# Performance work log

Measured on AMD Instinct MI355X. Metric: run time of the kernel, lower is better.

## Reference

```python
import jax, jax.numpy as jnp
import numpy as np

N, E, C, L, NG = 50000, 600000, 128, 7, 512
EPS = 1e-7


def layer_norm(z, g, b):
    mu = z.mean(-1, keepdims=True)
    var = ((z - mu) ** 2).mean(-1, keepdims=True)
    return (z - mu) * jax.lax.rsqrt(var + 1e-5) * g + b


def setup_inputs() -> dict:
    key = jax.random.key(0)
    ks = jax.random.split(key, 16)
    inp = {
        'x': jax.random.randint(ks[0], (N, 9), 0, 64, dtype=jnp.int32),
        'edge_index': jax.random.randint(ks[1], (2, E), 0, N, dtype=jnp.int32),
        'edge_attr': jax.random.randint(ks[2], (E, 3), 0, 8, dtype=jnp.int32),
        'batch': jnp.sort(jax.random.randint(ks[3], (N,), 0, NG, dtype=jnp.int32)),
        'atom_emb': jax.random.normal(ks[4], (9, 64, C), jnp.float32) * 0.1,
        'bond_emb': jax.random.normal(ks[5], (3, 8, C), jnp.float32) * 0.1,
        'vn_emb': jnp.zeros((1, C), jnp.float32),
        'conv_W1': jax.random.normal(ks[6], (L, C, 2 * C), jnp.float32) / np.sqrt(C),
        'conv_b1': jnp.zeros((L, 2 * C), jnp.float32),
        'conv_g1': jnp.ones((L, 2 * C), jnp.float32),
        'conv_bb1': jnp.zeros((L, 2 * C), jnp.float32),
        'conv_W2': jax.random.normal(ks[7], (L, 2 * C, C), jnp.float32) / np.sqrt(2 * C),
        'conv_b2': jnp.zeros((L, C), jnp.float32),
        'norm_g': jnp.ones((L, C), jnp.float32),
        'norm_b': jnp.zeros((L, C), jnp.float32),
        'vn_W1': jax.random.normal(ks[8], (L - 1, C, C), jnp.float32) / np.sqrt(C),
        'vn_b1': jnp.zeros((L - 1, C), jnp.float32),
        'vn_g': jnp.ones((L - 1, C), jnp.float32),
        'vn_bb': jnp.zeros((L - 1, C), jnp.float32),
        'vn_W2': jax.random.normal(ks[9], (L - 1, C, C), jnp.float32) / np.sqrt(C),
        'vn_b2': jnp.zeros((L - 1, C), jnp.float32),
    }
    return inp


def reference(x, edge_index, edge_attr, batch, atom_emb, bond_emb, vn_emb,
              conv_W1, conv_b1, conv_g1, conv_bb1, conv_W2, conv_b2,
              norm_g, norm_b, vn_W1, vn_b1, vn_g, vn_bb, vn_W2, vn_b2):
    src, dst = edge_index[0], edge_index[1]

    # AtomEncoder: sum of per-feature embeddings -> [N, C]
    h = atom_emb[jnp.arange(9), x].sum(axis=1)
    # BondEncoder (conv_encode_edge=False) -> [E, C]
    edge_emb = bond_emb[jnp.arange(3), edge_attr].sum(axis=1)

    # virtual node embedding (one per graph)
    vn = jnp.broadcast_to(vn_emb[0], (NG, C))
    h = h + vn[batch]

    def gen_conv(l, hx):
        # GENConv: msg = relu(x_j + e) + eps; softmax aggregation (t=1); MLP(x+m)
        msg = jax.nn.relu(hx[src] + edge_emb) + EPS                      # [E, C]
        mx = jax.ops.segment_max(msg, dst, num_segments=N)               # [N, C]
        e = jnp.exp(msg - mx[dst])
        den = jax.ops.segment_sum(e, dst, num_segments=N)
        m = jax.ops.segment_sum(msg * (e / (den[dst] + 1e-16)), dst, num_segments=N)
        z = hx + m
        z = jax.nn.relu(layer_norm(z @ conv_W1[l] + conv_b1[l], conv_g1[l], conv_bb1[l]))
        return z @ conv_W2[l] + conv_b2[l]

    # res+ block: Conv -> [Norm -> ReLU -> (VN update) -> Conv + res]*
    h = gen_conv(0, h)
    for l in range(1, L):
        h2 = jax.nn.relu(layer_norm(h, norm_g[l - 1], norm_b[l - 1]))
        vtmp = jax.ops.segment_sum(h2, batch, num_segments=NG) + vn
        v = jax.nn.relu(layer_norm(vtmp @ vn_W1[l - 1] + vn_b1[l - 1], vn_g[l - 1], vn_bb[l - 1]))
        vn = v @ vn_W2[l - 1] + vn_b2[l - 1]
        h2 = h2 + vn[batch]
        h = gen_conv(l, h2) + h
    h = layer_norm(h, norm_g[L - 1], norm_b[L - 1])

    # global_add_pool -> [NG, C]
    return jax.ops.segment_sum(h, batch, num_segments=NG)
```

## Files before the change

### kernel.cpp

```cpp
#include <hip/hip_runtime.h>
#include <hip/hip_bf16.h>
#include <stdint.h>

#define N_NODES 50000
#define N_EDGES 600000
#define CH 128
#define NLAYERS 7
#define NGRAPHS 512

typedef __hip_bfloat16 bf16;
using bf16x8 = __attribute__((ext_vector_type(8))) __bf16;
using f32x4  = __attribute__((ext_vector_type(4))) float;
using u32x4  = __attribute__((ext_vector_type(4))) uint32_t;

static __device__ __forceinline__ float b2f(bf16 v){ return __bfloat162float(v); }

static __device__ __forceinline__ void bar_lds(){
  asm volatile("s_waitcnt lgkmcnt(0)" ::: "memory");
  __builtin_amdgcn_sched_barrier(0);
  __builtin_amdgcn_s_barrier();
}

__global__ void k_detect(const uint32_t* __restrict__ g, int* __restrict__ flag){
  if (threadIdx.x == 0 && blockIdx.x == 0) flag[0] = (g[0] == 0x3F803F80u) ? 1 : 0;
}

struct Segs { const void* src[12]; float* dst[12]; int n[12]; };

__global__ void k_cvt_all(const int* __restrict__ flag, Segs S){
  int f = flag[0];
  int seg = blockIdx.y;
  int n = S.n[seg];
  const void* src = S.src[seg];
  float* dst = S.dst[seg];
  for (int i = blockIdx.x*blockDim.x + threadIdx.x; i < n; i += gridDim.x*blockDim.x)
    dst[i] = f ? b2f(((const bf16*)src)[i]) : ((const float*)src)[i];
}

__global__ void k_transpose_all(const int* __restrict__ flag,
    const void* W1, const void* W2, const void* vW1, const void* vW2,
    bf16* W1p, bf16* W2T, bf16* vW1p, bf16* vW2T){
  int f = flag[0];
  const int T0 = NLAYERS*128*256, T1 = NLAYERS*256*128;
  const int T2 = (NLAYERS-1)*128*128;
  int total = T0+T1+2*T2;
  for (int i = blockIdx.x*blockDim.x + threadIdx.x; i < total; i += gridDim.x*blockDim.x){
    float v;
    if (i < T0){
      int idx = i; int l = idx/(128*256); int rem = idx - l*128*256; int k = rem >> 8; int n = rem & 255;
      v = f ? b2f(((const bf16*)W1)[idx]) : ((const float*)W1)[idx];
      W1p[(size_t)l*256*128 + n*128 + (k ^ ((n&7)<<3))] = __float2bfloat16(v);
    } else if (i < T0+T1){
      int idx = i-T0; int l = idx/(256*128); int rem = idx - l*256*128; int k = rem >> 7; int n = rem & 127;
      v = f ? b2f(((const bf16*)W2)[idx]) : ((const float*)W2)[idx];
      W2T[(size_t)l*128*256 + n*256 + k] = __float2bfloat16(v);
    } else if (i < T0+T1+T2){
      int idx = i-T0-T1; int l = idx/(128*128); int rem = idx - l*128*128; int k = rem >> 7; int n = rem & 127;
      v = f ? b2f(((const bf16*)vW1)[idx]) : ((const float*)vW1)[idx];
      vW1p[(size_t)l*128*128 + n*128 + (k ^ ((n&7)<<3))] = __float2bfloat16(v);
    } else {
      int idx = i-T0-T1-T2; int l = idx/(128*128); int rem = idx - l*128*128; int k = rem >> 7; int n = rem & 127;
      v = f ? b2f(((const bf16*)vW2)[idx]) : ((const float*)vW2)[idx];
      vW2T[(size_t)l*128*128 + n*128 + k] = __float2bfloat16(v);
    }
  }
}

__global__ void k_bondC(const int* __restrict__ flag, const void* __restrict__ bond,
                        uint32_t* __restrict__ bondC){
  int i = blockIdx.x*blockDim.x + threadIdx.x;
  if (i >= 512*64) return;
  int f = flag[0];
  int idx = i >> 6, t = i & 63;
  int a0 = idx & 7, a1 = (idx>>3) & 7, a2 = (idx>>6) & 7;
  auto g = [&](int e)->float{ return f ? b2f(((const bf16*)bond)[e]) : ((const float*)bond)[e]; };
  int c0 = 2*t, c1 = 2*t+1;
  float s0 = g((0*8+a0)*128 + c0) + g((1*8+a1)*128 + c0) + g((2*8+a2)*128 + c0);
  float s1 = g((0*8+a0)*128 + c1) + g((1*8+a1)*128 + c1) + g((2*8+a2)*128 + c1);
  __hip_bfloat162 p; p.x = __float2bfloat16(s0); p.y = __float2bfloat16(s1);
  bondC[i] = *reinterpret_cast<uint32_t*>(&p);
}

__global__ void k_zero_i32(int* p, int n){
  for (int i = blockIdx.x*blockDim.x + threadIdx.x; i < n; i += gridDim.x*blockDim.x) p[i] = 0;
}

__global__ void k_hist(const int* __restrict__ keys, int* __restrict__ counts, int n){
  for (int i = blockIdx.x*blockDim.x + threadIdx.x; i < n; i += gridDim.x*blockDim.x)
    atomicAdd(&counts[keys[i]], 1);
}

__global__ __launch_bounds__(256) void k_scanA(const int* __restrict__ in, int* __restrict__ out,
                                               int* __restrict__ bsums, int n){
  __shared__ int lds[256];
  int t = threadIdx.x;
  int base = blockIdx.x * 1024;
  int v[4]; int s = 0;
  #pragma unroll
  for (int i=0;i<4;i++){ int idx = base + t*4 + i; int x = (idx<n)? in[idx] : 0; v[i]=x; s+=x; }
  lds[t] = s; __syncthreads();
  for (int off=1; off<256; off<<=1){
    int x = (t>=off)? lds[t-off] : 0;
    __syncthreads();
    lds[t] += x;
    __syncthreads();
  }
  int p = lds[t] - s;
  #pragma unroll
  for (int i=0;i<4;i++){ int idx = base + t*4 + i; if (idx<n) out[idx] = p; p += v[i]; }
  if (t==255) bsums[blockIdx.x] = lds[255];
}

__global__ __launch_bounds__(256) void k_scanB(int* bsums, int nblk){
  __shared__ int lds[256];
  int t = threadIdx.x;
  int v = (t<nblk)? bsums[t] : 0;
  lds[t] = v; __syncthreads();
  for (int off=1; off<256; off<<=1){
    int x = (t>=off)? lds[t-off] : 0;
    __syncthreads();
    lds[t] += x;
    __syncthreads();
  }
  if (t<nblk) bsums[t] = lds[t] - v;
}

__global__ void k_scanC(int* out, const int* bsums, int n){
  for (int i = blockIdx.x*blockDim.x + threadIdx.x; i < n; i += gridDim.x*blockDim.x)
    out[i] += bsums[i >> 10];
}

__global__ void k_scatter(const int* __restrict__ ei, const int* __restrict__ ea,
                          const int* __restrict__ row_ptr, int* __restrict__ fill,
                          uint32_t* __restrict__ csr){
  for (int e = blockIdx.x*blockDim.x + threadIdx.x; e < N_EDGES; e += gridDim.x*blockDim.x){
    int src = ei[e];
    int dst = ei[N_EDGES + e];
    int pos = row_ptr[dst] + atomicAdd(&fill[dst], 1);
    uint32_t a0 = (uint32_t)ea[e*3+0], a1 = (uint32_t)ea[e*3+1], a2 = (uint32_t)ea[e*3+2];
    csr[pos] = (uint32_t)src | ((a0 | (a1<<3) | (a2<<6)) << 16);
  }
}

__global__ void k_gptr(const int* __restrict__ batch, int* __restrict__ gptr){
  int i = blockIdx.x*blockDim.x + threadIdx.x;
  if (i >= N_NODES) return;
  int b = batch[i];
  if (i == 0){ for (int g=0; g<=b; ++g) gptr[g] = 0; }
  else { int bp = batch[i-1]; for (int g=bp+1; g<=b; ++g) gptr[g] = i; }
  if (i == N_NODES-1){ for (int g=b+1; g<=NGRAPHS; ++g) gptr[g] = N_NODES; }
}

__global__ __launch_bounds__(128) void k_atom_encode(const int* __restrict__ x,
    const float* __restrict__ atom_emb, const float* __restrict__ vn_emb,
    uint32_t* __restrict__ hxb){
  int n = blockIdx.x; int c = threadIdx.x;
  float s = vn_emb[c];
  #pragma unroll
  for (int f=0; f<9; ++f){
    int xv = x[n*9+f];
    s += atom_emb[(f*64 + xv)*CH + c];
  }
  float o = __shfl_xor(s, 1);
  if ((c & 1) == 0){
    __hip_bfloat162 p; p.x = __float2bfloat16(s); p.y = __float2bfloat16(o);
    hxb[n*64 + (c>>1)] = *reinterpret_cast<uint32_t*>(&p);
  }
}

__global__ void k_vn_init(const float* __restrict__ vn_emb, float* __restrict__ vn){
  for (int i = blockIdx.x*blockDim.x + threadIdx.x; i < NGRAPHS*CH; i += gridDim.x*blockDim.x)
    vn[i] = vn_emb[i & (CH-1)];
}

__global__ __launch_bounds__(64) void k_aggregate(const uint32_t* __restrict__ hxb,
     const uint32_t* __restrict__ csr, const int* __restrict__ row_ptr,
     const uint32_t* __restrict__ bondC, uint32_t* __restrict__ z){
  int n = (blockIdx.x & 7)*(N_NODES/8) + (blockIdx.x >> 3);
  int t = threadIdx.x;
  int s0 = row_ptr[n], s1 = row_ptr[n+1];
  float sa=0.f, sb=0.f, wa=0.f, wb=0.f;
  int i = s0;
  for (; i+4 <= s1; i += 4){
    uint32_t u0=csr[i], u1=csr[i+1], u2=csr[i+2], u3=csr[i+3];
    uint32_t h0 = hxb[(size_t)(u0 & 0xFFFFu)*64 + t];
    uint32_t h1 = hxb[(size_t)(u1 & 0xFFFFu)*64 + t];
    uint32_t h2 = hxb[(size_t)(u2 & 0xFFFFu)*64 + t];
    uint32_t h3 = hxb[(size_t)(u3 & 0xFFFFu)*64 + t];
    uint32_t c0 = bondC[(size_t)(u0 >> 16)*64 + t];
    uint32_t c1 = bondC[(size_t)(u1 >> 16)*64 + t];
    uint32_t c2 = bondC[(size_t)(u2 >> 16)*64 + t];
    uint32_t c3 = bondC[(size_t)(u3 >> 16)*64 + t];
    #define EDGE(hp, bc) { \
      float va = __uint_as_float(hp << 16) + __uint_as_float(bc << 16); \
      float vb = __uint_as_float(hp & 0xFFFF0000u) + __uint_as_float(bc & 0xFFFF0000u); \
      va = fmaxf(va, 0.f) + 1e-7f; vb = fmaxf(vb, 0.f) + 1e-7f; \
      float pa = __expf(va - 10.f), pb = __expf(vb - 10.f); \
      sa += pa; wa += pa*va; sb += pb; wb += pb*vb; }
    EDGE(h0, c0) EDGE(h1, c1) EDGE(h2, c2) EDGE(h3, c3)
  }
  for (; i < s1; ++i){
    uint32_t u = csr[i];
    uint32_t hp = hxb[(size_t)(u & 0xFFFFu)*64 + t];
    uint32_t bc = bondC[(size_t)(u >> 16)*64 + t];
    EDGE(hp, bc)
    #undef EDGE
  }
  uint32_t own = hxb[(size_t)n*64 + t];
  float za = __uint_as_float(own << 16)         + wa/(sa + 1e-16f);
  float zb = __uint_as_float(own & 0xFFFF0000u) + wb/(sb + 1e-16f);
  __hip_bfloat162 p; p.x = __float2bfloat16(za); p.y = __float2bfloat16(zb);
  z[(size_t)n*64 + (t ^ ((n&7)<<2))] = *reinterpret_cast<uint32_t*>(&p);
}

template<int K, int N1, int N2, bool VNIN, bool BF16IO>
__global__ __launch_bounds__(512, 2) void k_mlp12(const bf16* __restrict__ A,
    const float* __restrict__ Af32,
    const bf16* __restrict__ W1s,
    const float* __restrict__ b1, const float* __restrict__ g1, const float* __restrict__ bb1,
    const bf16* __restrict__ W2T,
    const float* __restrict__ b2,
    const float* __restrict__ lng, const float* __restrict__ lnb,
    const void* __restrict__ residual, void* __restrict__ out,
    bf16* __restrict__ hxn, int relu2, int M, int NT)
{
  constexpr int KK1 = K/32;
  constexpr int WC  = N1/4;
  constexpr int JC  = WC/16;
  constexpr int KK2 = N1/32;
  __shared__ __align__(16) bf16 W1L[N1*K];
  __shared__ __align__(16) bf16 AL[2][64*K];
  __shared__ __align__(16) bf16 zt[64*N1];
  __shared__ float lnp[64][4][2];
  __shared__ float lnv[64][2];

  const int tid = threadIdx.x;
  const int wid = tid >> 6, lane = tid & 63;
  const int wr = wid >> 2, wc = wid & 3;
  const int rlo = lane & 15, hi = lane >> 4, khi = hi*8;

  {
    constexpr int NC_ = (N1*K*2)/1024/8;
    #pragma unroll
    for (int c=0;c<NC_;++c){
      int cc = c*8 + wid;
      __builtin_amdgcn_global_load_lds((const uint32_t*)((const char*)W1s + cc*1024 + lane*16),
                                       (uint32_t*)((char*)W1L + cc*1024), 16, 0, 0);
    }
  }

  float b1v[JC], gv[JC], bbv[JC];
  #pragma unroll
  for (int jc=0;jc<JC;++jc){
    int col = wc*WC + jc*16 + rlo;
    b1v[jc] = b1[col]; gv[jc] = g1[col]; bbv[jc] = bb1[col];
  }
  float bv2[2] = { b2[wc*32 + rlo], b2[wc*32 + 16 + rlo] };
  float lngv[2] = {0.f,0.f}, lnbv[2] = {0.f,0.f};
  if (hxn){
    lngv[0] = lng[wc*32 + rlo];      lnbv[0] = lnb[wc*32 + rlo];
    lngv[1] = lng[wc*32 + 16 + rlo]; lnbv[1] = lnb[wc*32 + 16 + rlo];
  }
  u32x4 b2raw[2][KK2];
  #pragma unroll
  for (int ct=0;ct<2;++ct){
    const bf16* wp = W2T + (size_t)(wc*32 + ct*16 + rlo)*N1 + khi;
    #pragma unroll
    for (int kk=0;kk<KK2;++kk){
      b2raw[ct][kk] = *reinterpret_cast<const u32x4*>(wp + kk*32);
      asm volatile("" : "+v"(b2raw[ct][kk]));
    }
  }

  auto stageA = [&](int nb, int tile){
    if constexpr (!VNIN){
      const char* src = (const char*)A + (size_t)tile*(64*K*2);
      constexpr int NCA = (64*K*2)/1024/8;
      #pragma unroll
      for (int c=0;c<NCA;++c){
        int cc = c*8 + wid;
        __builtin_amdgcn_global_load_lds((const uint32_t*)(src + cc*1024 + lane*16),
                                         (uint32_t*)((char*)&AL[nb][0] + cc*1024), 16, 0, 0);
      }
    } else {
      int base = tile*64;
      #pragma unroll
      for (int e=0;e<(64*K/4)/512;++e){
        int idx = tid + e*512;
        int row = idx >> 5;
        int k4  = (idx & 31)*4;
        float4 v = *reinterpret_cast<const float4*>(Af32 + (size_t)(base+row)*K + k4);
        int s = (row&7)<<3;
        bf16* d = &AL[nb][row*K + (k4 ^ s)];
        d[0]=__float2bfloat16(v.x); d[1]=__float2bfloat16(v.y);
        d[2]=__float2bfloat16(v.z); d[3]=__float2bfloat16(v.w);
      }
    }
  };

  int t = blockIdx.x, buf = 0;
  stageA(0, t);
  __syncthreads();

  while (true){
    int tn = t + (int)gridDim.x;

    f32x4 acc1[2][JC];
    #pragma unroll
    for (int rt=0;rt<2;++rt)
      #pragma unroll
      for (int jc=0;jc<JC;++jc) acc1[rt][jc] = {0.f,0.f,0.f,0.f};
    #pragma unroll
    for (int kk=0;kk<KK1;++kk){
      bf16x8 af[2], bw[JC];
      #pragma unroll
      for (int rt=0;rt<2;++rt){
        int lr = wr*32 + rt*16 + rlo;
        af[rt] = *reinterpret_cast<const bf16x8*>(&AL[buf][lr*K + ((kk*32 + khi) ^ ((lr&7)<<3))]);
      }
      #pragma unroll
      for (int jc=0;jc<JC;++jc){
        int n = wc*WC + jc*16 + rlo;
        bw[jc] = *reinterpret_cast<const bf16x8*>(&W1L[n*K + ((kk*32 + khi) ^ ((n&7)<<3))]);
      }
      #pragma unroll
      for (int rt=0;rt<2;++rt)
        #pragma unroll
        for (int jc=0;jc<JC;++jc)
          acc1[rt][jc] = __builtin_amdgcn_mfma_f32_16x16x32_bf16(af[rt], bw[jc], acc1[rt][jc], 0,0,0);
    }

    if (tn < NT) stageA(buf^1, tn);
    float resv[2][2][4];
    if (residual){
      #pragma unroll
      for (int rt=0;rt<2;++rt)
        #pragma unroll
        for (int r=0;r<4;++r){
          int grow = t*64 + wr*32 + rt*16 + hi*4 + r; if (grow >= M) grow = M-1;
          #pragma unroll
          for (int ct=0;ct<2;++ct){
            size_t off = (size_t)grow*N2 + wc*32 + ct*16 + rlo;
            resv[rt][ct][r] = BF16IO ? b2f(((const bf16*)residual)[off])
                                     : ((const float*)residual)[off];
          }
        }
    }
    __builtin_amdgcn_sched_barrier(0);

    float p[2][4], q[2][4];
    #pragma unroll
    for (int rt=0;rt<2;++rt)
      #pragma unroll
      for (int r=0;r<4;++r){ p[rt][r]=0.f; q[rt][r]=0.f; }
    #pragma unroll
    for (int jc=0;jc<JC;++jc)
      #pragma unroll
      for (int rt=0;rt<2;++rt)
        #pragma unroll
        for (int r=0;r<4;++r){
          float v = acc1[rt][jc][r] + b1v[jc]; acc1[rt][jc][r] = v;
          p[rt][r] += v; q[rt][r] += v*v;
        }
    #pragma unroll
    for (int rt=0;rt<2;++rt)
      #pragma unroll
      for (int r=0;r<4;++r){
        float pv = p[rt][r], qv = q[rt][r];
        #pragma unroll
        for (int off=1; off<16; off<<=1){ pv += __shfl_xor(pv, off); qv += __shfl_xor(qv, off); }
        if (rlo == 0){
          int row = wr*32 + rt*16 + hi*4 + r;
          lnp[row][wc][0] = pv; lnp[row][wc][1] = qv;
        }
      }
    bar_lds();
    if (tid < 64){
      float P=0.f, Q=0.f;
      #pragma unroll
      for (int w=0;w<4;++w){ P += lnp[tid][w][0]; Q += lnp[tid][w][1]; }
      float mu = P*(1.f/N1);
      lnv[tid][0] = mu;
      lnv[tid][1] = rsqrtf(Q*(1.f/N1) - mu*mu + 1e-5f);
    }
    bar_lds();

    #pragma unroll
    for (int rt=0;rt<2;++rt)
      #pragma unroll
      for (int r=0;r<4;++r){
        int row = wr*32 + rt*16 + hi*4 + r;
        float mu = lnv[row][0], rs = lnv[row][1];
        #pragma unroll
        for (int jc=0;jc<JC;++jc){
          int col = wc*WC + jc*16 + rlo;
          float y = (acc1[rt][jc][r]-mu)*rs*gv[jc] + bbv[jc];
          zt[row*N1 + (col ^ ((row&7)<<3))] = __float2bfloat16(fmaxf(y, 0.f));
        }
      }
    bar_lds();

    f32x4 acc2[2][2];
    #pragma unroll
    for (int rt=0;rt<2;++rt)
      #pragma unroll
      for (int ct=0;ct<2;++ct) acc2[rt][ct] = {0.f,0.f,0.f,0.f};
    #pragma unroll
    for (int kk=0;kk<KK2;++kk){
      bf16x8 a2[2];
      #pragma unroll
      for (int rt=0;rt<2;++rt){
        int row = wr*32 + rt*16 + rlo;
        a2[rt] = *reinterpret_cast<const bf16x8*>(&zt[row*N1 + ((kk*32 + khi) ^ ((row&7)<<3))]);
      }
      #pragma unroll
      for (int rt=0;rt<2;++rt)
        #pragma unroll
        for (int ct=0;ct<2;++ct){
          bf16x8 bb;
          __builtin_memcpy(&bb, &b2raw[ct][kk], 16);
          acc2[rt][ct] = __builtin_amdgcn_mfma_f32_16x16x32_bf16(a2[rt], bb, acc2[rt][ct], 0,0,0);
        }
    }

    float vmat[2][2][4];
    #pragma unroll
    for (int rt=0;rt<2;++rt)
      #pragma unroll
      for (int ct=0;ct<2;++ct)
        #pragma unroll
        for (int r=0;r<4;++r){
          float v = acc2[rt][ct][r] + bv2[ct];
          if (residual) v += resv[rt][ct][r];
          vmat[rt][ct][r] = v;
          int grow = t*64 + wr*32 + rt*16 + hi*4 + r;
          if (grow < M){
            size_t off = (size_t)grow*N2 + wc*32 + ct*16 + rlo;
            if (BF16IO) ((bf16*)out)[off] = __float2bfloat16(v);
            else        ((float*)out)[off] = v;
          }
        }

    if (hxn){
      #pragma unroll
      for (int rt=0;rt<2;++rt)
        #pragma unroll
        for (int r=0;r<4;++r){
          float pv = vmat[rt][0][r] + vmat[rt][1][r];
          float qv = vmat[rt][0][r]*vmat[rt][0][r] + vmat[rt][1][r]*vmat[rt][1][r];
          #pragma unroll
          for (int off=1; off<16; off<<=1){ pv += __shfl_xor(pv, off); qv += __shfl_xor(qv, off); }
          if (rlo == 0){
            int row = wr*32 + rt*16 + hi*4 + r;
            lnp[row][wc][0] = pv; lnp[row][wc][1] = qv;
          }
        }
      bar_lds();
      if (tid < 64){
        float P=0.f, Q=0.f;
        #pragma unroll
        for (int w=0;w<4;++w){ P += lnp[tid][w][0]; Q += lnp[tid][w][1]; }
        float mu = P*(1.f/N2);
        lnv[tid][0] = mu;
        lnv[tid][1] = rsqrtf(Q*(1.f/N2) - mu*mu + 1e-5f);
      }
      bar_lds();
      #pragma unroll
      for (int rt=0;rt<2;++rt)
        #pragma unroll
        for (int r=0;r<4;++r){
          int row = wr*32 + rt*16 + hi*4 + r;
          float mu = lnv[row][0], rs = lnv[row][1];
          int grow = t*64 + row;
          if (grow < M){
            #pragma unroll
            for (int ct=0;ct<2;++ct){
              float y = (vmat[rt][ct][r]-mu)*rs*lngv[ct] + lnbv[ct];
              if (relu2) y = fmaxf(y, 0.f);
              hxn[(size_t)grow*N2 + wc*32 + ct*16 + rlo] = __float2bfloat16(y);
            }
          }
        }
    }

    if (tn >= NT) break;
    t = tn; buf ^= 1;
    __syncthreads();
  }
}

__global__ void k_vncopy(const float* __restrict__ vn, float* __restrict__ vnacc){
  int i = blockIdx.x*blockDim.x + threadIdx.x;
  if (i < NGRAPHS*CH) vnacc[i] = vn[i];
}

#define SEGC 128
__global__ __launch_bounds__(128) void k_segsum2(const bf16* __restrict__ hxn,
    const int* __restrict__ batch, float* __restrict__ vnacc){
  int c = threadIdx.x;
  int n0 = blockIdx.x*SEGC;
  int n1 = n0 + SEGC; if (n1 > N_NODES) n1 = N_NODES;
  if (n0 >= N_NODES) return;
  int cur = batch[n0];
  float s = 0.f;
  for (int n = n0; n < n1; ++n){
    int b = batch[n];
    if (b != cur){ atomicAdd(&vnacc[cur*CH + c], s); s = 0.f; cur = b; }
    s += b2f(hxn[(size_t)n*CH + c]);
  }
  atomicAdd(&vnacc[cur*CH + c], s);
}

__global__ void k_add_vn(const uint32_t* __restrict__ hxn, const float* __restrict__ vn,
                         const int* __restrict__ batch, uint32_t* __restrict__ hxb){
  for (int i = blockIdx.x*blockDim.x + threadIdx.x; i < N_NODES*64; i += gridDim.x*blockDim.x){
    int n = i >> 6; int t = i & 63;
    uint32_t hp = hxn[i];
    float2 vv = *reinterpret_cast<const float2*>(vn + (size_t)batch[n]*CH + 2*t);
    float za = __uint_as_float(hp << 16)         + vv.x;
    float zb = __uint_as_float(hp & 0xFFFF0000u) + vv.y;
    __hip_bfloat162 p; p.x = __float2bfloat16(za); p.y = __float2bfloat16(zb);
    hxb[i] = *reinterpret_cast<uint32_t*>(&p);
  }
}

__global__ __launch_bounds__(128) void k_pool(const bf16* __restrict__ hxn,
    const int* __restrict__ gptr, const int* __restrict__ flag, void* __restrict__ out){
  int g = blockIdx.x; int c = threadIdx.x;
  float s = 0.f;
  for (int n = gptr[g]; n < gptr[g+1]; ++n) s += b2f(hxn[(size_t)n*CH + c]);
  if (flag[0]) ((bf16*)out)[g*CH+c] = __float2bfloat16(s);
  else         ((float*)out)[g*CH+c] = s;
}

extern "C" void kernel_launch(void* const* d_in, const int* in_sizes, int n_in,
                              void* d_out, int out_size, void* d_ws, size_t ws_size,
                              hipStream_t stream)
{
  const int*  x     = (const int*) d_in[0];
  const int*  ei    = (const int*) d_in[1];
  const int*  ea    = (const int*) d_in[2];
  const int*  batch = (const int*) d_in[3];
  const void* atom_emb = d_in[4];
  const void* bond_emb = d_in[5];
  const void* vn_emb   = d_in[6];
  const void* conv_W1  = d_in[7];
  const void* conv_b1  = d_in[8];
  const void* conv_g1  = d_in[9];
  const void* conv_bb1 = d_in[10];
  const void* conv_W2  = d_in[11];
  const void* conv_b2  = d_in[12];
  const void* norm_g   = d_in[13];
  const void* norm_b   = d_in[14];
  const void* vn_W1    = d_in[15];
  const void* vn_b1    = d_in[16];
  const void* vn_g     = d_in[17];
  const void* vn_bb    = d_in[18];
  const void* vn_W2    = d_in[19];
  const void* vn_b2    = d_in[20];

  char* wsb = (char*)d_ws;
  size_t off = 0;
  auto alloc = [&](size_t bytes)->char*{ char* p = wsb + off; off += (bytes + 255) & ~(size_t)255; return p; };
  const int ZROWS = 50048;
  uint32_t* hb    = (uint32_t*)alloc(sizeof(uint32_t)*ZROWS*64);
  uint32_t* hxn   = (uint32_t*)alloc(sizeof(uint32_t)*ZROWS*64);
  uint32_t* hxb   = (uint32_t*)alloc(sizeof(uint32_t)*N_NODES*64);
  uint32_t* z     = (uint32_t*)alloc(sizeof(uint32_t)*ZROWS*64);
  float*    vn    = (float*)   alloc(sizeof(float)*NGRAPHS*CH);
  float*    vnacc = (float*)   alloc(sizeof(float)*NGRAPHS*CH);
  bf16*     W1Tp  = (bf16*)    alloc(sizeof(bf16)*NLAYERS*256*128);
  bf16*     W2T   = (bf16*)    alloc(sizeof(bf16)*NLAYERS*128*256);
  bf16*     vW1Tp = (bf16*)    alloc(sizeof(bf16)*(NLAYERS-1)*128*128);
  bf16*     vW2T  = (bf16*)    alloc(sizeof(bf16)*(NLAYERS-1)*128*128);
  int* row_ptr = (int*)alloc(sizeof(int)*(N_NODES+1));
  int* counts  = (int*)alloc(sizeof(int)*(N_NODES+1));
  uint32_t* csr = (uint32_t*)alloc(sizeof(uint32_t)*N_EDGES);
  int* gptr    = (int*)alloc(sizeof(int)*(NGRAPHS+1));
  int* bsums   = (int*)alloc(sizeof(int)*256);
  int* flag    = (int*)alloc(sizeof(int)*64);
  float* atomF = (float*)alloc(sizeof(float)*9*64*CH);
  uint32_t* bondC = (uint32_t*)alloc(sizeof(uint32_t)*512*64);
  float* vnEF  = (float*)alloc(sizeof(float)*CH);
  float* b1F   = (float*)alloc(sizeof(float)*NLAYERS*2*CH);
  float* g1F   = (float*)alloc(sizeof(float)*NLAYERS*2*CH);
  float* bb1F  = (float*)alloc(sizeof(float)*NLAYERS*2*CH);
  float* b2F   = (float*)alloc(sizeof(float)*NLAYERS*CH);
  float* ngF   = (float*)alloc(sizeof(float)*NLAYERS*CH);
  float* nbF   = (float*)alloc(sizeof(float)*NLAYERS*CH);
  float* vb1F  = (float*)alloc(sizeof(float)*(NLAYERS-1)*CH);
  float* vgF   = (float*)alloc(sizeof(float)*(NLAYERS-1)*CH);
  float* vbbF  = (float*)alloc(sizeof(float)*(NLAYERS-1)*CH);
  float* vb2F  = (float*)alloc(sizeof(float)*(NLAYERS-1)*CH);

  k_detect<<<1, 64, 0, stream>>>((const uint32_t*)norm_g, flag);
  Segs S;
  int si = 0;
  auto seg = [&](const void* s_, float* d_, int n_){ S.src[si]=s_; S.dst[si]=d_; S.n[si]=n_; ++si; };
  seg(atom_emb, atomF, 9*64*CH);
  seg(vn_emb,   vnEF,  CH);
  seg(conv_b1,  b1F,  NLAYERS*2*CH);
  seg(conv_g1,  g1F,  NLAYERS*2*CH);
  seg(conv_bb1, bb1F, NLAYERS*2*CH);
  seg(conv_b2,  b2F,  NLAYERS*CH);
  seg(norm_g,   ngF,  NLAYERS*CH);
  seg(norm_b,   nbF,  NLAYERS*CH);
  seg(vn_b1,    vb1F, (NLAYERS-1)*CH);
  seg(vn_g,     vgF,  (NLAYERS-1)*CH);
  seg(vn_bb,    vbbF, (NLAYERS-1)*CH);
  seg(vn_b2,    vb2F, (NLAYERS-1)*CH);
  k_cvt_all<<<dim3(72, 12), 256, 0, stream>>>(flag, S);
  k_transpose_all<<<640, 256, 0, stream>>>(flag, conv_W1, conv_W2, vn_W1, vn_W2,
                                           W1Tp, W2T, vW1Tp, vW2T);
  k_bondC<<<128, 256, 0, stream>>>(flag, bond_emb, bondC);

  k_zero_i32<<<64, 256, 0, stream>>>(counts, N_NODES+1);
  k_hist<<<512, 256, 0, stream>>>(ei + N_EDGES, counts, N_EDGES);
  int nblkE = (N_NODES+1 + 1023)/1024;
  k_scanA<<<nblkE, 256, 0, stream>>>(counts, row_ptr, bsums, N_NODES+1);
  k_scanB<<<1, 256, 0, stream>>>(bsums, nblkE);
  k_scanC<<<64, 256, 0, stream>>>(row_ptr, bsums, N_NODES+1);
  k_zero_i32<<<64, 256, 0, stream>>>(counts, N_NODES+1);
  k_scatter<<<512, 256, 0, stream>>>(ei, ea, row_ptr, counts, csr);
  k_gptr<<<(N_NODES+255)/256, 256, 0, stream>>>(batch, gptr);

  k_atom_encode<<<N_NODES, 128, 0, stream>>>(x, atomF, vnEF, hxb);
  k_vn_init<<<64, 256, 0, stream>>>(vnEF, vn);

  const int NT_CONV = (N_NODES + 63)/64;
  const int NT_VN   = NGRAPHS/64;

  for (int l = 0; l < NLAYERS; ++l){
    if (l > 0){
      k_vncopy<<<(NGRAPHS*CH+255)/256, 256, 0, stream>>>(vn, vnacc);
      k_segsum2<<<(N_NODES+SEGC-1)/SEGC, 128, 0, stream>>>((const bf16*)hxn, batch, vnacc);
      k_mlp12<128,128,128,true,false><<<NT_VN, 512, 0, stream>>>(nullptr, vnacc,
          vW1Tp + (size_t)(l-1)*128*128, vb1F + (l-1)*CH, vgF + (l-1)*CH, vbbF + (l-1)*CH,
          vW2T + (size_t)(l-1)*128*128, vb2F + (l-1)*CH,
          nullptr, nullptr, nullptr, vn, nullptr, 0, NGRAPHS, NT_VN);
      k_add_vn<<<1024, 256, 0, stream>>>(hxn, vn, batch, hxb);
    }
    k_aggregate<<<N_NODES, 64, 0, stream>>>(hxb, csr, row_ptr, bondC, z);
    k_mlp12<128,256,128,false,true><<<256, 512, 0, stream>>>((const bf16*)z, nullptr,
        W1Tp + (size_t)l*256*128, b1F + l*2*CH, g1F + l*2*CH, bb1F + l*2*CH,
        W2T + (size_t)l*128*256, b2F + l*CH,
        ngF + l*CH, nbF + l*CH,
        (l==0)? nullptr : (const void*)hb, (void*)hb, (bf16*)hxn,
        (l < NLAYERS-1) ? 1 : 0, N_NODES, NT_CONV);
  }
  k_pool<<<NGRAPHS, 128, 0, stream>>>((const bf16*)hxn, gptr, flag, d_out);
}
```

Before: 952.6 us.

## Fuse edge softmax aggregation into the conv MLP kernel

The separate per-node aggregation kernel is removed. Each 64-row tile of the conv MLP kernel now computes its own softmax-weighted neighbour aggregation directly into shared memory, with 8 rows per wave, before running the two GEMMs and layernorms. This drops the z intermediate write and read and one launch per layer. In exchange, the gather latency is no longer overlapped by a double-buffered A stage, and the 256 persistent blocks at 2 per CU may hide memory latency less well than the old 50000 small blocks. The VN MLP path is split off into its own simplified kernel.

```diff
diff --git a/kernel.cpp b/kernel.cpp
--- a/kernel.cpp
+++ b/kernel.cpp
@@ -173,56 +173,290 @@
     vn[i] = vn_emb[i & (CH-1)];
 }
 
-__global__ __launch_bounds__(64) void k_aggregate(const uint32_t* __restrict__ hxb,
-     const uint32_t* __restrict__ csr, const int* __restrict__ row_ptr,
-     const uint32_t* __restrict__ bondC, uint32_t* __restrict__ z){
-  int n = (blockIdx.x & 7)*(N_NODES/8) + (blockIdx.x >> 3);
-  int t = threadIdx.x;
-  int s0 = row_ptr[n], s1 = row_ptr[n+1];
-  float sa=0.f, sb=0.f, wa=0.f, wb=0.f;
-  int i = s0;
-  for (; i+4 <= s1; i += 4){
-    uint32_t u0=csr[i], u1=csr[i+1], u2=csr[i+2], u3=csr[i+3];
-    uint32_t h0 = hxb[(size_t)(u0 & 0xFFFFu)*64 + t];
-    uint32_t h1 = hxb[(size_t)(u1 & 0xFFFFu)*64 + t];
-    uint32_t h2 = hxb[(size_t)(u2 & 0xFFFFu)*64 + t];
-    uint32_t h3 = hxb[(size_t)(u3 & 0xFFFFu)*64 + t];
-    uint32_t c0 = bondC[(size_t)(u0 >> 16)*64 + t];
-    uint32_t c1 = bondC[(size_t)(u1 >> 16)*64 + t];
-    uint32_t c2 = bondC[(size_t)(u2 >> 16)*64 + t];
-    uint32_t c3 = bondC[(size_t)(u3 >> 16)*64 + t];
-    #define EDGE(hp, bc) { \
-      float va = __uint_as_float(hp << 16) + __uint_as_float(bc << 16); \
-      float vb = __uint_as_float(hp & 0xFFFF0000u) + __uint_as_float(bc & 0xFFFF0000u); \
-      va = fmaxf(va, 0.f) + 1e-7f; vb = fmaxf(vb, 0.f) + 1e-7f; \
-      float pa = __expf(va - 10.f), pb = __expf(vb - 10.f); \
-      sa += pa; wa += pa*va; sb += pb; wb += pb*vb; }
-    EDGE(h0, c0) EDGE(h1, c1) EDGE(h2, c2) EDGE(h3, c3)
-  }
-  for (; i < s1; ++i){
-    uint32_t u = csr[i];
-    uint32_t hp = hxb[(size_t)(u & 0xFFFFu)*64 + t];
-    uint32_t bc = bondC[(size_t)(u >> 16)*64 + t];
-    EDGE(hp, bc)
-    #undef EDGE
-  }
-  uint32_t own = hxb[(size_t)n*64 + t];
-  float za = __uint_as_float(own << 16)         + wa/(sa + 1e-16f);
-  float zb = __uint_as_float(own & 0xFFFF0000u) + wb/(sb + 1e-16f);
-  __hip_bfloat162 p; p.x = __float2bfloat16(za); p.y = __float2bfloat16(zb);
-  z[(size_t)n*64 + (t ^ ((n&7)<<2))] = *reinterpret_cast<uint32_t*>(&p);
-}
-
-template<int K, int N1, int N2, bool VNIN, bool BF16IO>
-__global__ __launch_bounds__(512, 2) void k_mlp12(const bf16* __restrict__ A,
-    const float* __restrict__ Af32,
+template<int K, int N1, int N2>
+__global__ __launch_bounds__(512, 2) void k_mlp13(
+    const uint32_t* __restrict__ hxb,
+    const uint32_t* __restrict__ csr, const int* __restrict__ row_ptr,
+    const uint32_t* __restrict__ bondC,
     const bf16* __restrict__ W1s,
     const float* __restrict__ b1, const float* __restrict__ g1, const float* __restrict__ bb1,
     const bf16* __restrict__ W2T,
     const float* __restrict__ b2,
     const float* __restrict__ lng, const float* __restrict__ lnb,
-    const void* __restrict__ residual, void* __restrict__ out,
+    const bf16* __restrict__ residual, bf16* __restrict__ out,
     bf16* __restrict__ hxn, int relu2, int M, int NT)
+{
+  constexpr int KK1 = K/32;
+  constexpr int WC  = N1/4;
+  constexpr int JC  = WC/16;
+  constexpr int KK2 = N1/32;
+  __shared__ __align__(16) bf16 W1L[N1*K];
+  __shared__ __align__(16) bf16 AL[64*K];
+  __shared__ __align__(16) bf16 zt[64*N1];
+  __shared__ float lnp[64][4][2];
+  __shared__ float lnv[64][2];
+
+  const int tid = threadIdx.x;
+  const int wid = tid >> 6, lane = tid & 63;
+  const int wr = wid >> 2, wc = wid & 3;
+  const int rlo = lane & 15, hi = lane >> 4, khi = hi*8;
+
+  {
+    constexpr int NC_ = (N1*K*2)/1024/8;
+    #pragma unroll
+    for (int c=0;c<NC_;++c){
+      int cc = c*8 + wid;
+      __builtin_amdgcn_global_load_lds((const uint32_t*)((const char*)W1s + cc*1024 + lane*16),
+                                       (uint32_t*)((char*)W1L + cc*1024), 16, 0, 0);
+    }
+  }
+
+  float b1v[JC], gv[JC], bbv[JC];
+  #pragma unroll
+  for (int jc=0;jc<JC;++jc){
+    int col = wc*WC + jc*16 + rlo;
+    b1v[jc] = b1[col]; gv[jc] = g1[col]; bbv[jc] = bb1[col];
+  }
+  float bv2[2] = { b2[wc*32 + rlo], b2[wc*32 + 16 + rlo] };
+  float lngv[2] = { lng[wc*32 + rlo], lng[wc*32 + 16 + rlo] };
+  float lnbv[2] = { lnb[wc*32 + rlo], lnb[wc*32 + 16 + rlo] };
+  u32x4 b2raw[2][KK2];
+  #pragma unroll
+  for (int ct=0;ct<2;++ct){
+    const bf16* wp = W2T + (size_t)(wc*32 + ct*16 + rlo)*N1 + khi;
+    #pragma unroll
+    for (int kk=0;kk<KK2;++kk){
+      b2raw[ct][kk] = *reinterpret_cast<const u32x4*>(wp + kk*32);
+      asm volatile("" : "+v"(b2raw[ct][kk]));
+    }
+  }
+
+  uint32_t* AL32 = (uint32_t*)AL;
+
+  for (int t = blockIdx.x; ; t += (int)gridDim.x){
+    #pragma unroll 1
+    for (int j=0;j<8;++j){
+      int row = wid*8 + j;
+      int n = t*64 + row;
+      uint32_t res = 0;
+      if (n < M){
+        int s0 = row_ptr[n], s1 = row_ptr[n+1];
+        float sa=0.f, sb=0.f, wa=0.f, wb=0.f;
+        int i = s0;
+        for (; i+4 <= s1; i += 4){
+          uint32_t u0=csr[i], u1=csr[i+1], u2=csr[i+2], u3=csr[i+3];
+          uint32_t h0 = hxb[(size_t)(u0 & 0xFFFFu)*64 + lane];
+          uint32_t h1 = hxb[(size_t)(u1 & 0xFFFFu)*64 + lane];
+          uint32_t h2 = hxb[(size_t)(u2 & 0xFFFFu)*64 + lane];
+          uint32_t h3 = hxb[(size_t)(u3 & 0xFFFFu)*64 + lane];
+          uint32_t c0 = bondC[(size_t)(u0 >> 16)*64 + lane];
+          uint32_t c1 = bondC[(size_t)(u1 >> 16)*64 + lane];
+          uint32_t c2 = bondC[(size_t)(u2 >> 16)*64 + lane];
+          uint32_t c3 = bondC[(size_t)(u3 >> 16)*64 + lane];
+          #define EDGE(hp, bc) { \
+            float va = __uint_as_float(hp << 16) + __uint_as_float(bc << 16); \
+            float vb = __uint_as_float(hp & 0xFFFF0000u) + __uint_as_float(bc & 0xFFFF0000u); \
+            va = fmaxf(va, 0.f) + 1e-7f; vb = fmaxf(vb, 0.f) + 1e-7f; \
+            float pa = __expf(va - 10.f), pb = __expf(vb - 10.f); \
+            sa += pa; wa += pa*va; sb += pb; wb += pb*vb; }
+          EDGE(h0, c0) EDGE(h1, c1) EDGE(h2, c2) EDGE(h3, c3)
+        }
+        for (; i < s1; ++i){
+          uint32_t u = csr[i];
+          uint32_t hp = hxb[(size_t)(u & 0xFFFFu)*64 + lane];
+          uint32_t bc = bondC[(size_t)(u >> 16)*64 + lane];
+          EDGE(hp, bc)
+          #undef EDGE
+        }
+        uint32_t own = hxb[(size_t)n*64 + lane];
+        float za = __uint_as_float(own << 16)         + wa/(sa + 1e-16f);
+        float zb = __uint_as_float(own & 0xFFFF0000u) + wb/(sb + 1e-16f);
+        __hip_bfloat162 p; p.x = __float2bfloat16(za); p.y = __float2bfloat16(zb);
+        res = *reinterpret_cast<uint32_t*>(&p);
+      }
+      AL32[row*(K/2) + (lane ^ ((row&7)<<2))] = res;
+    }
+    __syncthreads();
+
+    f32x4 acc1[2][JC];
+    #pragma unroll
+    for (int rt=0;rt<2;++rt)
+      #pragma unroll
+      for (int jc=0;jc<JC;++jc) acc1[rt][jc] = {0.f,0.f,0.f,0.f};
+    #pragma unroll
+    for (int kk=0;kk<KK1;++kk){
+      bf16x8 af[2], bw[JC];
+      #pragma unroll
+      for (int rt=0;rt<2;++rt){
+        int lr = wr*32 + rt*16 + rlo;
+        af[rt] = *reinterpret_cast<const bf16x8*>(&AL[lr*K + ((kk*32 + khi) ^ ((lr&7)<<3))]);
+      }
+      #pragma unroll
+      for (int jc=0;jc<JC;++jc){
+        int n = wc*WC + jc*16 + rlo;
+        bw[jc] = *reinterpret_cast<const bf16x8*>(&W1L[n*K + ((kk*32 + khi) ^ ((n&7)<<3))]);
+      }
+      #pragma unroll
+      for (int rt=0;rt<2;++rt)
+        #pragma unroll
+        for (int jc=0;jc<JC;++jc)
+          acc1[rt][jc] = __builtin_amdgcn_mfma_f32_16x16x32_bf16(af[rt], bw[jc], acc1[rt][jc], 0,0,0);
+    }
+
+    float resv[2][2][4];
+    if (residual){
+      #pragma unroll
+      for (int rt=0;rt<2;++rt)
+        #pragma unroll
+        for (int r=0;r<4;++r){
+          int grow = t*64 + wr*32 + rt*16 + hi*4 + r; if (grow >= M) grow = M-1;
+          #pragma unroll
+          for (int ct=0;ct<2;++ct)
+            resv[rt][ct][r] = b2f(residual[(size_t)grow*N2 + wc*32 + ct*16 + rlo]);
+        }
+    }
+    __builtin_amdgcn_sched_barrier(0);
+
+    float p[2][4], q[2][4];
+    #pragma unroll
+    for (int rt=0;rt<2;++rt)
+      #pragma unroll
+      for (int r=0;r<4;++r){ p[rt][r]=0.f; q[rt][r]=0.f; }
+    #pragma unroll
+    for (int jc=0;jc<JC;++jc)
+      #pragma unroll
+      for (int rt=0;rt<2;++rt)
+        #pragma unroll
+        for (int r=0;r<4;++r){
+          float v = acc1[rt][jc][r] + b1v[jc]; acc1[rt][jc][r] = v;
+          p[rt][r] += v; q[rt][r] += v*v;
+        }
+    #pragma unroll
+    for (int rt=0;rt<2;++rt)
+      #pragma unroll
+      for (int r=0;r<4;++r){
+        float pv = p[rt][r], qv = q[rt][r];
+        #pragma unroll
+        for (int off=1; off<16; off<<=1){ pv += __shfl_xor(pv, off); qv += __shfl_xor(qv, off); }
+        if (rlo == 0){
+          int row = wr*32 + rt*16 + hi*4 + r;
+          lnp[row][wc][0] = pv; lnp[row][wc][1] = qv;
+        }
+      }
+    bar_lds();
+    if (tid < 64){
+      float P=0.f, Q=0.f;
+      #pragma unroll
+      for (int w=0;w<4;++w){ P += lnp[tid][w][0]; Q += lnp[tid][w][1]; }
+      float mu = P*(1.f/N1);
+      lnv[tid][0] = mu;
+      lnv[tid][1] = rsqrtf(Q*(1.f/N1) - mu*mu + 1e-5f);
+    }
+    bar_lds();
+
+    #pragma unroll
+    for (int rt=0;rt<2;++rt)
+      #pragma unroll
+      for (int r=0;r<4;++r){
+        int row = wr*32 + rt*16 + hi*4 + r;
+        float mu = lnv[row][0], rs = lnv[row][1];
+        #pragma unroll
+        for (int jc=0;jc<JC;++jc){
+          int col = wc*WC + jc*16 + rlo;
+          float y = (acc1[rt][jc][r]-mu)*rs*gv[jc] + bbv[jc];
+          zt[row*N1 + (col ^ ((row&7)<<3))] = __float2bfloat16(fmaxf(y, 0.f));
+        }
+      }
+    bar_lds();
+
+    f32x4 acc2[2][2];
+    #pragma unroll
+    for (int rt=0;rt<2;++rt)
+      #pragma unroll
+      for (int ct=0;ct<2;++ct) acc2[rt][ct] = {0.f,0.f,0.f,0.f};
+    #pragma unroll
+    for (int kk=0;kk<KK2;++kk){
+      bf16x8 a2[2];
+      #pragma unroll
+      for (int rt=0;rt<2;++rt){
+        int row = wr*32 + rt*16 + rlo;
+        a2[rt] = *reinterpret_cast<const bf16x8*>(&zt[row*N1 + ((kk*32 + khi) ^ ((row&7)<<3))]);
+      }
+      #pragma unroll
+      for (int rt=0;rt<2;++rt)
+        #pragma unroll
+        for (int ct=0;ct<2;++ct){
+          bf16x8 bb;
+          __builtin_memcpy(&bb, &b2raw[ct][kk], 16);
+          acc2[rt][ct] = __builtin_amdgcn_mfma_f32_16x16x32_bf16(a2[rt], bb, acc2[rt][ct], 0,0,0);
+        }
+    }
+
+    float vmat[2][2][4];
+    #pragma unroll
+    for (int rt=0;rt<2;++rt)
+      #pragma unroll
+      for (int ct=0;ct<2;++ct)
+        #pragma unroll
+        for (int r=0;r<4;++r){
+          float v = acc2[rt][ct][r] + bv2[ct];
+          if (residual) v += resv[rt][ct][r];
+          vmat[rt][ct][r] = v;
+          int grow = t*64 + wr*32 + rt*16 + hi*4 + r;
+          if (grow < M) out[(size_t)grow*N2 + wc*32 + ct*16 + rlo] = __float2bfloat16(v);
+        }
+
+    #pragma unroll
+    for (int rt=0;rt<2;++rt)
+      #pragma unroll
+      for (int r=0;r<4;++r){
+        float pv = vmat[rt][0][r] + vmat[rt][1][r];
+        float qv = vmat[rt][0][r]*vmat[rt][0][r] + vmat[rt][1][r]*vmat[rt][1][r];
+        #pragma unroll
+        for (int off=1; off<16; off<<=1){ pv += __shfl_xor(pv, off); qv += __shfl_xor(qv, off); }
+        if (rlo == 0){
+          int row = wr*32 + rt*16 + hi*4 + r;
+          lnp[row][wc][0] = pv; lnp[row][wc][1] = qv;
+        }
+      }
+    bar_lds();
+    if (tid < 64){
+      float P=0.f, Q=0.f;
+      #pragma unroll
+      for (int w=0;w<4;++w){ P += lnp[tid][w][0]; Q += lnp[tid][w][1]; }
+      float mu = P*(1.f/N2);
+      lnv[tid][0] = mu;
+      lnv[tid][1] = rsqrtf(Q*(1.f/N2) - mu*mu + 1e-5f);
+    }
+    bar_lds();
+    #pragma unroll
+    for (int rt=0;rt<2;++rt)
+      #pragma unroll
+      for (int r=0;r<4;++r){
+        int row = wr*32 + rt*16 + hi*4 + r;
+        float mu = lnv[row][0], rs = lnv[row][1];
+        int grow = t*64 + row;
+        if (grow < M){
+          #pragma unroll
+          for (int ct=0;ct<2;++ct){
+            float y = (vmat[rt][ct][r]-mu)*rs*lngv[ct] + lnbv[ct];
+            if (relu2) y = fmaxf(y, 0.f);
+            hxn[(size_t)grow*N2 + wc*32 + ct*16 + rlo] = __float2bfloat16(y);
+          }
+        }
+      }
+
+    if (t + (int)gridDim.x >= NT) break;
+    __syncthreads();
+  }
+}
+
+template<int K, int N1, int N2>
+__global__ __launch_bounds__(512, 2) void k_mlpvn(const float* __restrict__ Af32,
+    const bf16* __restrict__ W1s,
+    const float* __restrict__ b1, const float* __restrict__ g1, const float* __restrict__ bb1,
+    const bf16* __restrict__ W2T, const float* __restrict__ b2,
+    float* __restrict__ out, int M, int NT)
 {
   constexpr int KK1 = K/32;
   constexpr int WC  = N1/4;
@@ -248,7 +482,6 @@
                                        (uint32_t*)((char*)W1L + cc*1024), 16, 0, 0);
     }
   }
-
   float b1v[JC], gv[JC], bbv[JC];
   #pragma unroll
   for (int jc=0;jc<JC;++jc){
@@ -256,11 +489,6 @@
     b1v[jc] = b1[col]; gv[jc] = g1[col]; bbv[jc] = bb1[col];
   }
   float bv2[2] = { b2[wc*32 + rlo], b2[wc*32 + 16 + rlo] };
-  float lngv[2] = {0.f,0.f}, lnbv[2] = {0.f,0.f};
-  if (hxn){
-    lngv[0] = lng[wc*32 + rlo];      lnbv[0] = lnb[wc*32 + rlo];
-    lngv[1] = lng[wc*32 + 16 + rlo]; lnbv[1] = lnb[wc*32 + 16 + rlo];
-  }
   u32x4 b2raw[2][KK2];
   #pragma unroll
   for (int ct=0;ct<2;++ct){
@@ -273,28 +501,17 @@
   }
 
   auto stageA = [&](int nb, int tile){
-    if constexpr (!VNIN){
-      const char* src = (const char*)A + (size_t)tile*(64*K*2);
-      constexpr int NCA = (64*K*2)/1024/8;
-      #pragma unroll
-      for (int c=0;c<NCA;++c){
-        int cc = c*8 + wid;
-        __builtin_amdgcn_global_load_lds((const uint32_t*)(src + cc*1024 + lane*16),
-                                         (uint32_t*)((char*)&AL[nb][0] + cc*1024), 16, 0, 0);
-      }
-    } else {
-      int base = tile*64;
-      #pragma unroll
-      for (int e=0;e<(64*K/4)/512;++e){
-        int idx = tid + e*512;
-        int row = idx >> 5;
-        int k4  = (idx & 31)*4;
-        float4 v = *reinterpret_cast<const float4*>(Af32 + (size_t)(base+row)*K + k4);
-        int s = (row&7)<<3;
-        bf16* d = &AL[nb][row*K + (k4 ^ s)];
-        d[0]=__float2bfloat16(v.x); d[1]=__float2bfloat16(v.y);
-        d[2]=__float2bfloat16(v.z); d[3]=__float2bfloat16(v.w);
-      }
+    int base = tile*64;
+    #pragma unroll
+    for (int e=0;e<(64*K/4)/512;++e){
+      int idx = tid + e*512;
+      int row = idx >> 5;
+      int k4  = (idx & 31)*4;
+      float4 v = *reinterpret_cast<const float4*>(Af32 + (size_t)(base+row)*K + k4);
+      int s = (row&7)<<3;
+      bf16* d = &AL[nb][row*K + (k4 ^ s)];
+      d[0]=__float2bfloat16(v.x); d[1]=__float2bfloat16(v.y);
+      d[2]=__float2bfloat16(v.z); d[3]=__float2bfloat16(v.w);
     }
   };
 
@@ -304,7 +521,6 @@
 
   while (true){
     int tn = t + (int)gridDim.x;
-
     f32x4 acc1[2][JC];
     #pragma unroll
     for (int rt=0;rt<2;++rt)
@@ -329,23 +545,7 @@
         for (int jc=0;jc<JC;++jc)
           acc1[rt][jc] = __builtin_amdgcn_mfma_f32_16x16x32_bf16(af[rt], bw[jc], acc1[rt][jc], 0,0,0);
     }
-
     if (tn < NT) stageA(buf^1, tn);
-    float resv[2][2][4];
-    if (residual){
-      #pragma unroll
-      for (int rt=0;rt<2;++rt)
-        #pragma unroll
-        for (int r=0;r<4;++r){
-          int grow = t*64 + wr*32 + rt*16 + hi*4 + r; if (grow >= M) grow = M-1;
-          #pragma unroll
-          for (int ct=0;ct<2;++ct){
-            size_t off = (size_t)grow*N2 + wc*32 + ct*16 + rlo;
-            resv[rt][ct][r] = BF16IO ? b2f(((const bf16*)residual)[off])
-                                     : ((const float*)residual)[off];
-          }
-        }
-    }
     __builtin_amdgcn_sched_barrier(0);
 
     float p[2][4], q[2][4];
@@ -384,7 +584,6 @@
       lnv[tid][1] = rsqrtf(Q*(1.f/N1) - mu*mu + 1e-5f);
     }
     bar_lds();
-
     #pragma unroll
     for (int rt=0;rt<2;++rt)
       #pragma unroll
@@ -422,66 +621,16 @@
           acc2[rt][ct] = __builtin_amdgcn_mfma_f32_16x16x32_bf16(a2[rt], bb, acc2[rt][ct], 0,0,0);
         }
     }
-
-    float vmat[2][2][4];
     #pragma unroll
     for (int rt=0;rt<2;++rt)
       #pragma unroll
       for (int ct=0;ct<2;++ct)
         #pragma unroll
         for (int r=0;r<4;++r){
-          float v = acc2[rt][ct][r] + bv2[ct];
-          if (residual) v += resv[rt][ct][r];
-          vmat[rt][ct][r] = v;
           int grow = t*64 + wr*32 + rt*16 + hi*4 + r;
-          if (grow < M){
-            size_t off = (size_t)grow*N2 + wc*32 + ct*16 + rlo;
-            if (BF16IO) ((bf16*)out)[off] = __float2bfloat16(v);
-            else        ((float*)out)[off] = v;
-          }
-        }
-
-    if (hxn){
-      #pragma unroll
-      for (int rt=0;rt<2;++rt)
-        #pragma unroll
-        for (int r=0;r<4;++r){
-          float pv = vmat[rt][0][r] + vmat[rt][1][r];
-          float qv = vmat[rt][0][r]*vmat[rt][0][r] + vmat[rt][1][r]*vmat[rt][1][r];
-          #pragma unroll
-          for (int off=1; off<16; off<<=1){ pv += __shfl_xor(pv, off); qv += __shfl_xor(qv, off); }
-          if (rlo == 0){
-            int row = wr*32 + rt*16 + hi*4 + r;
-            lnp[row][wc][0] = pv; lnp[row][wc][1] = qv;
-          }
-        }
-      bar_lds();
-      if (tid < 64){
-        float P=0.f, Q=0.f;
-        #pragma unroll
-        for (int w=0;w<4;++w){ P += lnp[tid][w][0]; Q += lnp[tid][w][1]; }
-        float mu = P*(1.f/N2);
-        lnv[tid][0] = mu;
-        lnv[tid][1] = rsqrtf(Q*(1.f/N2) - mu*mu + 1e-5f);
-      }
-      bar_lds();
-      #pragma unroll
-      for (int rt=0;rt<2;++rt)
-        #pragma unroll
-        for (int r=0;r<4;++r){
-          int row = wr*32 + rt*16 + hi*4 + r;
-          float mu = lnv[row][0], rs = lnv[row][1];
-          int grow = t*64 + row;
-          if (grow < M){
-            #pragma unroll
-            for (int ct=0;ct<2;++ct){
-              float y = (vmat[rt][ct][r]-mu)*rs*lngv[ct] + lnbv[ct];
-              if (relu2) y = fmaxf(y, 0.f);
-              hxn[(size_t)grow*N2 + wc*32 + ct*16 + rlo] = __float2bfloat16(y);
-            }
-          }
-        }
-    }
+          if (grow < M)
+            out[(size_t)grow*N2 + wc*32 + ct*16 + rlo] = acc2[rt][ct][r] + bv2[ct];
+        }
 
     if (tn >= NT) break;
     t = tn; buf ^= 1;
@@ -566,7 +715,6 @@
   uint32_t* hb    = (uint32_t*)alloc(sizeof(uint32_t)*ZROWS*64);
   uint32_t* hxn   = (uint32_t*)alloc(sizeof(uint32_t)*ZROWS*64);
   uint32_t* hxb   = (uint32_t*)alloc(sizeof(uint32_t)*N_NODES*64);
-  uint32_t* z     = (uint32_t*)alloc(sizeof(uint32_t)*ZROWS*64);
   float*    vn    = (float*)   alloc(sizeof(float)*NGRAPHS*CH);
   float*    vnacc = (float*)   alloc(sizeof(float)*NGRAPHS*CH);
   bf16*     W1Tp  = (bf16*)    alloc(sizeof(bf16)*NLAYERS*256*128);
@@ -634,18 +782,16 @@
     if (l > 0){
       k_vncopy<<<(NGRAPHS*CH+255)/256, 256, 0, stream>>>(vn, vnacc);
       k_segsum2<<<(N_NODES+SEGC-1)/SEGC, 128, 0, stream>>>((const bf16*)hxn, batch, vnacc);
-      k_mlp12<128,128,128,true,false><<<NT_VN, 512, 0, stream>>>(nullptr, vnacc,
+      k_mlpvn<128,128,128><<<NT_VN, 512, 0, stream>>>(vnacc,
           vW1Tp + (size_t)(l-1)*128*128, vb1F + (l-1)*CH, vgF + (l-1)*CH, vbbF + (l-1)*CH,
-          vW2T + (size_t)(l-1)*128*128, vb2F + (l-1)*CH,
-          nullptr, nullptr, nullptr, vn, nullptr, 0, NGRAPHS, NT_VN);
+          vW2T + (size_t)(l-1)*128*128, vb2F + (l-1)*CH, vn, NGRAPHS, NT_VN);
       k_add_vn<<<1024, 256, 0, stream>>>(hxn, vn, batch, hxb);
     }
-    k_aggregate<<<N_NODES, 64, 0, stream>>>(hxb, csr, row_ptr, bondC, z);
-    k_mlp12<128,256,128,false,true><<<256, 512, 0, stream>>>((const bf16*)z, nullptr,
+    k_mlp13<128,256,128><<<256, 512, 0, stream>>>(hxb, csr, row_ptr, bondC,
         W1Tp + (size_t)l*256*128, b1F + l*2*CH, g1F + l*2*CH, bb1F + l*2*CH,
         W2T + (size_t)l*128*256, b2F + l*CH,
         ngF + l*CH, nbF + l*CH,
-        (l==0)? nullptr : (const void*)hb, (void*)hb, (bf16*)hxn,
+        (l==0)? nullptr : (const bf16*)hb, (bf16*)hb, (bf16*)hxn,
         (l < NLAYERS-1) ? 1 : 0, N_NODES, NT_CONV);
   }
   k_pool<<<NGRAPHS, 128, 0, stream>>>((const bf16*)hxn, gptr, flag, d_out);
```

Measured after the change: 1.619 ms. 69.9% more time.

## Pack four nodes per aggregate block, unroll edges by eight, segment-sum per graph

Applied to the files above, without the earlier changes.

The aggregate kernel now runs four nodes per 256-thread block (one wave each) and adds an 8-edge unrolled loop that issues all gathers before the math, raising memory-level parallelism. The blockIdx node interleaving across 8 chunks is dropped, so node order per block becomes sequential. The virtual-node segment sum is replaced by one block per graph that walks the precomputed graph pointer range and folds in the previous vn, removing the copy kernel and the atomics. The per-graph loop may be imbalanced and offers only 512 blocks.

```diff
diff --git a/kernel.cpp b/kernel.cpp
--- a/kernel.cpp
+++ b/kernel.cpp
@@ -173,39 +173,49 @@
     vn[i] = vn_emb[i & (CH-1)];
 }
 
-__global__ __launch_bounds__(64) void k_aggregate(const uint32_t* __restrict__ hxb,
+__global__ __launch_bounds__(256) void k_aggregate(const uint32_t* __restrict__ hxb,
      const uint32_t* __restrict__ csr, const int* __restrict__ row_ptr,
      const uint32_t* __restrict__ bondC, uint32_t* __restrict__ z){
-  int n = (blockIdx.x & 7)*(N_NODES/8) + (blockIdx.x >> 3);
-  int t = threadIdx.x;
+  int n = blockIdx.x*4 + (threadIdx.x >> 6);
+  int t = threadIdx.x & 63;
   int s0 = row_ptr[n], s1 = row_ptr[n+1];
   float sa=0.f, sb=0.f, wa=0.f, wb=0.f;
   int i = s0;
+  #define EDGE(hp, bc) { \
+    float va = __uint_as_float(hp << 16) + __uint_as_float(bc << 16); \
+    float vb = __uint_as_float(hp & 0xFFFF0000u) + __uint_as_float(bc & 0xFFFF0000u); \
+    va = fmaxf(va, 0.f) + 1e-7f; vb = fmaxf(vb, 0.f) + 1e-7f; \
+    float pa = __expf(va - 10.f), pb = __expf(vb - 10.f); \
+    sa += pa; wa += pa*va; sb += pb; wb += pb*vb; }
+  for (; i+8 <= s1; i += 8){
+    uint32_t u[8], h[8], c[8];
+    #pragma unroll
+    for (int e=0;e<8;++e) u[e] = csr[i+e];
+    #pragma unroll
+    for (int e=0;e<8;++e) h[e] = hxb[(size_t)(u[e] & 0xFFFFu)*64 + t];
+    #pragma unroll
+    for (int e=0;e<8;++e) c[e] = bondC[(size_t)(u[e] >> 16)*64 + t];
+    #pragma unroll
+    for (int e=0;e<8;++e) EDGE(h[e], c[e])
+  }
   for (; i+4 <= s1; i += 4){
-    uint32_t u0=csr[i], u1=csr[i+1], u2=csr[i+2], u3=csr[i+3];
-    uint32_t h0 = hxb[(size_t)(u0 & 0xFFFFu)*64 + t];
-    uint32_t h1 = hxb[(size_t)(u1 & 0xFFFFu)*64 + t];
-    uint32_t h2 = hxb[(size_t)(u2 & 0xFFFFu)*64 + t];
-    uint32_t h3 = hxb[(size_t)(u3 & 0xFFFFu)*64 + t];
-    uint32_t c0 = bondC[(size_t)(u0 >> 16)*64 + t];
-    uint32_t c1 = bondC[(size_t)(u1 >> 16)*64 + t];
-    uint32_t c2 = bondC[(size_t)(u2 >> 16)*64 + t];
-    uint32_t c3 = bondC[(size_t)(u3 >> 16)*64 + t];
-    #define EDGE(hp, bc) { \
-      float va = __uint_as_float(hp << 16) + __uint_as_float(bc << 16); \
-      float vb = __uint_as_float(hp & 0xFFFF0000u) + __uint_as_float(bc & 0xFFFF0000u); \
-      va = fmaxf(va, 0.f) + 1e-7f; vb = fmaxf(vb, 0.f) + 1e-7f; \
-      float pa = __expf(va - 10.f), pb = __expf(vb - 10.f); \
-      sa += pa; wa += pa*va; sb += pb; wb += pb*vb; }
-    EDGE(h0, c0) EDGE(h1, c1) EDGE(h2, c2) EDGE(h3, c3)
+    uint32_t u[4], h[4], c[4];
+    #pragma unroll
+    for (int e=0;e<4;++e) u[e] = csr[i+e];
+    #pragma unroll
+    for (int e=0;e<4;++e) h[e] = hxb[(size_t)(u[e] & 0xFFFFu)*64 + t];
+    #pragma unroll
+    for (int e=0;e<4;++e) c[e] = bondC[(size_t)(u[e] >> 16)*64 + t];
+    #pragma unroll
+    for (int e=0;e<4;++e) EDGE(h[e], c[e])
   }
   for (; i < s1; ++i){
     uint32_t u = csr[i];
     uint32_t hp = hxb[(size_t)(u & 0xFFFFu)*64 + t];
     uint32_t bc = bondC[(size_t)(u >> 16)*64 + t];
     EDGE(hp, bc)
-    #undef EDGE
-  }
+  }
+  #undef EDGE
   uint32_t own = hxb[(size_t)n*64 + t];
   float za = __uint_as_float(own << 16)         + wa/(sa + 1e-16f);
   float zb = __uint_as_float(own & 0xFFFF0000u) + wb/(sb + 1e-16f);
@@ -489,26 +499,13 @@
   }
 }
 
-__global__ void k_vncopy(const float* __restrict__ vn, float* __restrict__ vnacc){
-  int i = blockIdx.x*blockDim.x + threadIdx.x;
-  if (i < NGRAPHS*CH) vnacc[i] = vn[i];
-}
-
-#define SEGC 128
-__global__ __launch_bounds__(128) void k_segsum2(const bf16* __restrict__ hxn,
-    const int* __restrict__ batch, float* __restrict__ vnacc){
-  int c = threadIdx.x;
-  int n0 = blockIdx.x*SEGC;
-  int n1 = n0 + SEGC; if (n1 > N_NODES) n1 = N_NODES;
-  if (n0 >= N_NODES) return;
-  int cur = batch[n0];
-  float s = 0.f;
-  for (int n = n0; n < n1; ++n){
-    int b = batch[n];
-    if (b != cur){ atomicAdd(&vnacc[cur*CH + c], s); s = 0.f; cur = b; }
-    s += b2f(hxn[(size_t)n*CH + c]);
-  }
-  atomicAdd(&vnacc[cur*CH + c], s);
+__global__ __launch_bounds__(128) void k_segsum_vn(const bf16* __restrict__ hxn,
+    const int* __restrict__ gptr, const float* __restrict__ vn, float* __restrict__ vnacc){
+  int g = blockIdx.x; int c = threadIdx.x;
+  float s = vn[g*CH + c];
+  int n0 = gptr[g], n1 = gptr[g+1];
+  for (int n = n0; n < n1; ++n) s += b2f(hxn[(size_t)n*CH + c]);
+  vnacc[g*CH + c] = s;
 }
 
 __global__ void k_add_vn(const uint32_t* __restrict__ hxn, const float* __restrict__ vn,
@@ -632,15 +629,14 @@
 
   for (int l = 0; l < NLAYERS; ++l){
     if (l > 0){
-      k_vncopy<<<(NGRAPHS*CH+255)/256, 256, 0, stream>>>(vn, vnacc);
-      k_segsum2<<<(N_NODES+SEGC-1)/SEGC, 128, 0, stream>>>((const bf16*)hxn, batch, vnacc);
+      k_segsum_vn<<<NGRAPHS, 128, 0, stream>>>((const bf16*)hxn, gptr, vn, vnacc);
       k_mlp12<128,128,128,true,false><<<NT_VN, 512, 0, stream>>>(nullptr, vnacc,
           vW1Tp + (size_t)(l-1)*128*128, vb1F + (l-1)*CH, vgF + (l-1)*CH, vbbF + (l-1)*CH,
           vW2T + (size_t)(l-1)*128*128, vb2F + (l-1)*CH,
           nullptr, nullptr, nullptr, vn, nullptr, 0, NGRAPHS, NT_VN);
       k_add_vn<<<1024, 256, 0, stream>>>(hxn, vn, batch, hxb);
     }
-    k_aggregate<<<N_NODES, 64, 0, stream>>>(hxb, csr, row_ptr, bondC, z);
+    k_aggregate<<<N_NODES/4, 256, 0, stream>>>(hxb, csr, row_ptr, bondC, z);
     k_mlp12<128,256,128,false,true><<<256, 512, 0, stream>>>((const bf16*)z, nullptr,
         W1Tp + (size_t)l*256*128, b1F + l*2*CH, g1F + l*2*CH, bb1F + l*2*CH,
         W2T + (size_t)l*128*256, b2F + l*CH,
```

New measurement: 982.7 us. 1.03x slower.
